# Optimization experiments

Hardware: AMD Instinct MI355X
Metric: run time of the kernel (lower is better)

The kernel has to match this reference:

```python
import jax, jax.numpy as jnp
import numpy as np
from jax import lax

NUM_GROUPS = 16
EPS = 1e-5  # PyTorch GroupNorm default
POOL = 2
CLAMP_MIN, CLAMP_MAX = 0.0, 1.0


def setup_inputs() -> dict:
    key = jax.random.key(0)
    ks = jax.random.split(key, 6)
    B, Cin, H, W = 32, 64, 128, 128
    Cout, K = 128, 3
    return {
        "x": jax.random.normal(ks[0], (B, Cin, H, W), dtype=jnp.float32),
        "conv_w": jax.random.normal(ks[1], (Cout, Cin, K, K), dtype=jnp.float32),
        "conv_b": jax.random.normal(ks[2], (Cout,), dtype=jnp.float32),
        "gn_w": jax.random.normal(ks[3], (Cout,), dtype=jnp.float32),
        "gn_b": jax.random.normal(ks[4], (Cout,), dtype=jnp.float32),
        "scale": jax.random.normal(ks[5], (Cout, 1, 1), dtype=jnp.float32),
    }


def reference(x, conv_w, conv_b, gn_w, gn_b, scale):
    # Conv2d, stride 1, no padding (PyTorch default): [B,Cout,H-2,W-2]
    y = lax.conv_general_dilated(
        x, conv_w, window_strides=(1, 1), padding="VALID",
        dimension_numbers=("NCHW", "OIHW", "NCHW"))
    y = y + conv_b[None, :, None, None]

    # GroupNorm over (C/G, H, W) per sample and group
    B, C, H, W = y.shape
    yg = y.reshape(B, NUM_GROUPS, C // NUM_GROUPS, H, W)
    mean = jnp.mean(yg, axis=(2, 3, 4), keepdims=True)
    var = jnp.var(yg, axis=(2, 3, 4), keepdims=True)
    yn = ((yg - mean) * lax.rsqrt(var + EPS)).reshape(B, C, H, W)
    yn = yn * gn_w[None, :, None, None] + gn_b[None, :, None, None]

    # channel-wise scale (scale shape [C,1,1])
    yn = yn * scale[None, :, :, :]

    # MaxPool2d(kernel=2, stride=2)
    p = lax.reduce_window(yn, -jnp.inf, lax.max,
                          (1, 1, POOL, POOL), (1, 1, POOL, POOL), "VALID")

    # clamp
    return jnp.clip(p, CLAMP_MIN, CLAMP_MAX)
```

## Files before the change

kernel.cpp:

```cpp
#include <hip/hip_runtime.h>
#include <hip/hip_fp16.h>

#define CIN   64
#define COUT  128
#define HIN   128
#define WIN   128
#define HOUT  126
#define WOUT  126
#define HP    63
#define WP    63
#define NB    32
#define NG    16
#define EPS   1e-5f
#define KTOT  576

#define CELLB 80
#define NCOLT 66
#define ROWB  (NCOLT * CELLB)
#define XHALF (4 * ROWB)
#define NTILE 126

#define YCHUNK 128
#define YPLANE (126 * YCHUNK)

typedef __attribute__((ext_vector_type(8))) _Float16 half8;
typedef __attribute__((ext_vector_type(4))) float f32x4;

__global__ __launch_bounds__(256) void wprep_kernel(
    const float* __restrict__ cw, ushort* __restrict__ wh, ushort* __restrict__ wl)
{
    int idx = blockIdx.x * 256 + threadIdx.x;
    if (idx >= COUT * KTOT) return;
    int co = idx / KTOT, k = idx - co * KTOT;
    int khw = k >> 6, ci = k & 63;
    float v = cw[(co * CIN + ci) * 9 + khw];
    __half h = __float2half(v);
    __half l = __float2half(v - __half2float(h));
    wh[idx] = __half_as_ushort(h);
    wl[idx] = __half_as_ushort(l);
}

__global__ __launch_bounds__(512, 4) void conv_mfma_kernel(
    const float* __restrict__ x, const ushort* __restrict__ wt_hi,
    const ushort* __restrict__ wt_lo, const float* __restrict__ cb,
    float* __restrict__ y, float* __restrict__ partials)
{
    __shared__ char xs[2 * XHALF];
    __shared__ float wred[8][4][2];

    const int tid = threadIdx.x;
    const int bid = blockIdx.x;
    const int w   = (bid & 7) * 504 + (bid >> 3);
    const int b   = w / 126;
    const int r   = w - b * 126;
    const int rp  = r >> 1;
    const int ct  = r & 1;
    const int r0x = rp * 2;

    const int l = tid & 63, wid = tid >> 6;
    const int l15 = l & 15, lhi = l >> 4;

    f32x4 acc[8];
#pragma unroll
    for (int nt = 0; nt < 8; ++nt) acc[nt] = (f32x4){0.f, 0.f, 0.f, 0.f};

    const float* xb = x + (size_t)b * (CIN * HIN * WIN);

    const int c4 = tid & 15, rr = (tid >> 4) & 3, cig = tid >> 6;
    const float* xmain = xb + (size_t)(cig * 4) * (HIN * WIN)
                       + (r0x + rr) * WIN + ct * 64 + c4 * 4;
    char* wmain = xs + rr * ROWB + (c4 * 4) * CELLB + cig * 8;

#define LOADMAIN(cip, f)                                                   \
    {                                                                      \
        _Pragma("unroll")                                                  \
        for (int q = 0; q < 4; ++q)                                        \
            f[q] = *(const f32x4*)(xmain + (size_t)((cip) * 32 + q) * (HIN * WIN)); \
    }

#define WRITEMAIN(f, buf)                                                  \
    {                                                                      \
        _Pragma("unroll")                                                  \
        for (int j = 0; j < 4; ++j) {                                      \
            ushort h0 = __half_as_ushort(__float2half(f[0][j]));           \
            ushort h1 = __half_as_ushort(__float2half(f[1][j]));           \
            ushort h2 = __half_as_ushort(__float2half(f[2][j]));           \
            ushort h3 = __half_as_ushort(__float2half(f[3][j]));           \
            uint2 hp;                                                      \
            hp.x = (unsigned)h0 | ((unsigned)h1 << 16);                    \
            hp.y = (unsigned)h2 | ((unsigned)h3 << 16);                    \
            *(uint2*)(wmain + (buf) * XHALF + j * CELLB) = hp;             \
        }                                                                  \
    }

#define TAIL(cip, buf)                                                     \
    if (tid < 32) {                                                        \
        int trr = tid & 3, tcig = tid >> 2;                                \
        float2 g[4];                                                       \
        _Pragma("unroll")                                                  \
        for (int q = 0; q < 4; ++q) {                                      \
            if (ct == 0)                                                   \
                g[q] = *(const float2*)(xb                                 \
                      + (size_t)((cip) * 32 + tcig * 4 + q) * (HIN * WIN)  \
                      + (r0x + trr) * WIN + 64);                           \
            else g[q] = make_float2(0.f, 0.f);                             \
        }                                                                  \
        _Pragma("unroll")                                                  \
        for (int j = 0; j < 2; ++j) {                                      \
            float v0 = j ? g[0].y : g[0].x, v1 = j ? g[1].y : g[1].x;      \
            float v2 = j ? g[2].y : g[2].x, v3 = j ? g[3].y : g[3].x;      \
            uint2 hp;                                                      \
            hp.x = (unsigned)__half_as_ushort(__float2half(v0))            \
                 | ((unsigned)__half_as_ushort(__float2half(v1)) << 16);   \
            hp.y = (unsigned)__half_as_ushort(__float2half(v2))            \
                 | ((unsigned)__half_as_ushort(__float2half(v3)) << 16);   \
            *(uint2*)(xs + (buf) * XHALF + trr * ROWB + (64 + j) * CELLB   \
                      + tcig * 8) = hp;                                    \
        }                                                                  \
    }

    const ushort* wbh = wt_hi + (size_t)(wid * 16 + l15) * KTOT + lhi * 8;
    const ushort* wbl = wt_lo + (size_t)(wid * 16 + l15) * KTOT + lhi * 8;
    const char* pb = xs + l15 * CELLB + lhi * 16;

#define COMPUTE(buf, cip)                                                  \
    {                                                                      \
        _Pragma("unroll")                                                  \
        for (int khw = 0; khw < 9; ++khw) {                                \
            const int kh = khw / 3, kw = khw - kh * 3;                     \
            half8 wh_ = *(const half8*)(wbh + khw * 64 + (cip) * 32);      \
            half8 wl_ = *(const half8*)(wbl + khw * 64 + (cip) * 32);      \
            half8 bv[8];                                                   \
            _Pragma("unroll")                                              \
            for (int nt = 0; nt < 8; ++nt)                                 \
                bv[nt] = *(const half8*)(pb + (buf) * XHALF                \
                        + ((nt >> 2) + kh) * ROWB                          \
                        + ((nt & 3) * 16 + kw) * CELLB);                   \
            _Pragma("unroll")                                              \
            for (int nt = 0; nt < 8; ++nt)                                 \
                acc[nt] = __builtin_amdgcn_mfma_f32_16x16x32_f16(          \
                    wh_, bv[nt], acc[nt], 0, 0, 0);                        \
            _Pragma("unroll")                                              \
            for (int nt = 0; nt < 8; ++nt)                                 \
                acc[nt] = __builtin_amdgcn_mfma_f32_16x16x32_f16(          \
                    wl_, bv[nt], acc[nt], 0, 0, 0);                        \
        }                                                                  \
    }

    {
        f32x4 f0[4];
        LOADMAIN(0, f0);
        WRITEMAIN(f0, 0);
        TAIL(0, 0);
    }
    __syncthreads();

    {
        f32x4 f1[4];
        LOADMAIN(1, f1);
        __builtin_amdgcn_sched_barrier(0);
        COMPUTE(0, 0);
        WRITEMAIN(f1, 1);
        TAIL(1, 1);
    }
    __syncthreads();
    COMPUTE(1, 1);

#undef LOADMAIN
#undef WRITEMAIN
#undef TAIL
#undef COMPUTE

    float cbv[4];
#pragma unroll
    for (int r2 = 0; r2 < 4; ++r2)
        cbv[r2] = cb[wid * 16 + lhi * 4 + r2];

    float* ybase = y + (size_t)b * COUT * YPLANE
                 + (size_t)((rp * 2 + ct) * YCHUNK) + l15;

    float s1 = 0.f, s2 = 0.f;
#pragma unroll
    for (int r2 = 0; r2 < 4; ++r2) {
        int co = wid * 16 + lhi * 4 + r2;
        float* yp = ybase + (size_t)co * YPLANE;
#pragma unroll
        for (int nt = 0; nt < 8; ++nt) {
            float v = acc[nt][r2] + cbv[r2];
            yp[(nt >> 2) * 64 + (nt & 3) * 16] = v;
            if (ct * 64 + (nt & 3) * 16 + l15 < WOUT) { s1 += v; s2 += v * v; }
        }
    }
#pragma unroll
    for (int d = 1; d < 16; d <<= 1) {
        s1 += __shfl_xor(s1, d);
        s2 += __shfl_xor(s2, d);
    }
    if (l15 == 0) {
        wred[wid][lhi][0] = s1;
        wred[wid][lhi][1] = s2;
    }
    __syncthreads();

    if (tid < NG) {
        int g = tid;
        int gw = g >> 1, h = g & 1;
        float t1 = wred[gw][h * 2][0] + wred[gw][h * 2 + 1][0];
        float t2 = wred[gw][h * 2][1] + wred[gw][h * 2 + 1][1];
        size_t pidx = (((size_t)b * NG + g) * NTILE + (rp * 2 + ct)) * 2;
        partials[pidx + 0] = t1;
        partials[pidx + 1] = t2;
    }
}

__global__ void stats_kernel(const float* __restrict__ partials,
                             float* __restrict__ stats)
{
    int t = blockIdx.x * blockDim.x + threadIdx.x;
    if (t >= NB * NG) return;
    float s1 = 0.f, s2 = 0.f;
    for (int j = 0; j < NTILE; ++j) {
        s1 += partials[((size_t)t * NTILE + j) * 2 + 0];
        s2 += partials[((size_t)t * NTILE + j) * 2 + 1];
    }
    const float N = 8.f * HOUT * WOUT;
    float mean = s1 / N;
    float var = s2 / N - mean * mean;
    stats[t * 2 + 0] = mean;
    stats[t * 2 + 1] = rsqrtf(var + EPS);
}

__global__ __launch_bounds__(256) void pool_kernel(
    const float* __restrict__ y, const float* __restrict__ stats,
    const float* __restrict__ gw, const float* __restrict__ gb,
    const float* __restrict__ sc, float* __restrict__ out)
{
    int idx = blockIdx.x * 256 + threadIdx.x;
    if (idx >= NB * COUT * HP * WP) return;
    int owp = idx % WP;
    int t = idx / WP;
    int ohp = t % HP; t /= HP;
    int c = t % COUT;
    int b = t / COUT;
    int g = c >> 3;

    float mean = stats[(b * NG + g) * 2 + 0];
    float rstd = stats[(b * NG + g) * 2 + 1];
    float ga = rstd * gw[c] * sc[c];
    float gbb = (gb[c] - mean * rstd * gw[c]) * sc[c];

    int ct = owp >> 5, col = (2 * owp) & 63;
    const float* yp = y + (size_t)(b * COUT + c) * YPLANE
                    + (ohp * 2 + ct) * YCHUNK + col;
    float2 r0 = *reinterpret_cast<const float2*>(yp);
    float2 r1 = *reinterpret_cast<const float2*>(yp + 64);
    float v0 = fmaf(r0.x, ga, gbb);
    float v1 = fmaf(r0.y, ga, gbb);
    float v2 = fmaf(r1.x, ga, gbb);
    float v3 = fmaf(r1.y, ga, gbb);
    float m = fmaxf(fmaxf(v0, v1), fmaxf(v2, v3));
    out[idx] = fminf(fmaxf(m, 0.f), 1.f);
}

extern "C" void kernel_launch(void* const* d_in, const int* in_sizes, int n_in,
                              void* d_out, int out_size, void* d_ws, size_t ws_size,
                              hipStream_t stream)
{
    const float* x  = (const float*)d_in[0];
    const float* cw = (const float*)d_in[1];
    const float* cbias = (const float*)d_in[2];
    const float* gw = (const float*)d_in[3];
    const float* gb = (const float*)d_in[4];
    const float* sc = (const float*)d_in[5];
    float* out = (float*)d_out;

    const size_t YSZ = (size_t)NB * COUT * YPLANE;
    float* y        = (float*)d_ws;
    float* partials = y + YSZ;
    float* stats    = partials + (size_t)NB * NG * NTILE * 2;
    ushort* wh      = (ushort*)(stats + 1024);
    ushort* wl      = wh + (size_t)COUT * KTOT;

    hipLaunchKernelGGL(wprep_kernel, dim3((COUT * KTOT + 255) / 256), dim3(256),
                       0, stream, cw, wh, wl);

    hipLaunchKernelGGL(conv_mfma_kernel, dim3(4032), dim3(512), 0, stream,
                       x, wh, wl, cbias, y, partials);

    hipLaunchKernelGGL(stats_kernel, dim3(2), dim3(256), 0, stream,
                       partials, stats);

    int total = NB * COUT * HP * WP;
    hipLaunchKernelGGL(pool_kernel, dim3((total + 255) / 256), dim3(256), 0, stream,
                       y, stats, gw, gb, sc, out);
}
```

Measured before the change: 285.8 us.

## Switch conv MFMA from 16x16x32 to 32x32x16 tiles with regrouped warps

Each wavefront now computes a 32-output-channel by 32-column tile with two 32x32x16 f16 MFMA accumulators (one per output row), replacing eight 16x16x32 accumulators. Waves are paired so each pair shares a channel group and splits the columns. The epilogue remaps the output layout and reduces GroupNorm partial sums per 8-channel group across the whole wave. The aim is to cut LDS operand loads per MFMA and make the matrix cores more efficient; the risk is a different LDS bank-access pattern and extra shuffle reductions.

New measurement: 397.9 us. 39.2% more time.

```diff
diff --git a/kernel.cpp b/kernel.cpp
--- a/kernel.cpp
+++ b/kernel.cpp
@@ -23,8 +23,9 @@
 #define YCHUNK 128
 #define YPLANE (126 * YCHUNK)
 
-typedef __attribute__((ext_vector_type(8))) _Float16 half8;
-typedef __attribute__((ext_vector_type(4))) float f32x4;
+typedef __attribute__((ext_vector_type(8)))  _Float16 half8;
+typedef __attribute__((ext_vector_type(4)))  float f32x4;
+typedef __attribute__((ext_vector_type(16))) float f32x16;
 
 __global__ __launch_bounds__(256) void wprep_kernel(
     const float* __restrict__ cw, ushort* __restrict__ wh, ushort* __restrict__ wl)
@@ -58,11 +59,13 @@
     const int r0x = rp * 2;
 
     const int l = tid & 63, wid = tid >> 6;
-    const int l15 = l & 15, lhi = l >> 4;
-
-    f32x4 acc[8];
-#pragma unroll
-    for (int nt = 0; nt < 8; ++nt) acc[nt] = (f32x4){0.f, 0.f, 0.f, 0.f};
+    const int wg = wid >> 1;
+    const int h  = wid & 1;
+    const int l31 = l & 31, lh = l >> 5;
+
+    f32x16 acc0 = (f32x16){0.f,0.f,0.f,0.f,0.f,0.f,0.f,0.f,
+                           0.f,0.f,0.f,0.f,0.f,0.f,0.f,0.f};
+    f32x16 acc1 = acc0;
 
     const float* xb = x + (size_t)b * (CIN * HIN * WIN);
 
@@ -119,31 +122,28 @@
         }                                                                  \
     }
 
-    const ushort* wbh = wt_hi + (size_t)(wid * 16 + l15) * KTOT + lhi * 8;
-    const ushort* wbl = wt_lo + (size_t)(wid * 16 + l15) * KTOT + lhi * 8;
-    const char* pb = xs + l15 * CELLB + lhi * 16;
+    const ushort* wbh = wt_hi + (size_t)(wg * 32 + l31) * KTOT + lh * 8;
+    const ushort* wbl = wt_lo + (size_t)(wg * 32 + l31) * KTOT + lh * 8;
+    const char* pb = xs + (h * 32 + l31) * CELLB + lh * 16;
 
 #define COMPUTE(buf, cip)                                                  \
     {                                                                      \
         _Pragma("unroll")                                                  \
         for (int khw = 0; khw < 9; ++khw) {                                \
             const int kh = khw / 3, kw = khw - kh * 3;                     \
-            half8 wh_ = *(const half8*)(wbh + khw * 64 + (cip) * 32);      \
-            half8 wl_ = *(const half8*)(wbl + khw * 64 + (cip) * 32);      \
-            half8 bv[8];                                                   \
             _Pragma("unroll")                                              \
-            for (int nt = 0; nt < 8; ++nt)                                 \
-                bv[nt] = *(const half8*)(pb + (buf) * XHALF                \
-                        + ((nt >> 2) + kh) * ROWB                          \
-                        + ((nt & 3) * 16 + kw) * CELLB);                   \
-            _Pragma("unroll")                                              \
-            for (int nt = 0; nt < 8; ++nt)                                 \
-                acc[nt] = __builtin_amdgcn_mfma_f32_16x16x32_f16(          \
-                    wh_, bv[nt], acc[nt], 0, 0, 0);                        \
-            _Pragma("unroll")                                              \
-            for (int nt = 0; nt < 8; ++nt)                                 \
-                acc[nt] = __builtin_amdgcn_mfma_f32_16x16x32_f16(          \
-                    wl_, bv[nt], acc[nt], 0, 0, 0);                        \
+            for (int k16 = 0; k16 < 2; ++k16) {                            \
+                half8 wh_ = *(const half8*)(wbh + khw * 64 + (cip) * 32 + k16 * 16); \
+                half8 wl_ = *(const half8*)(wbl + khw * 64 + (cip) * 32 + k16 * 16); \
+                half8 bv0 = *(const half8*)(pb + (buf) * XHALF             \
+                            + kh * ROWB + kw * CELLB + k16 * 32);          \
+                half8 bv1 = *(const half8*)(pb + (buf) * XHALF             \
+                            + (1 + kh) * ROWB + kw * CELLB + k16 * 32);    \
+                acc0 = __builtin_amdgcn_mfma_f32_32x32x16_f16(wh_, bv0, acc0, 0, 0, 0); \
+                acc1 = __builtin_amdgcn_mfma_f32_32x32x16_f16(wh_, bv1, acc1, 0, 0, 0); \
+                acc0 = __builtin_amdgcn_mfma_f32_32x32x16_f16(wl_, bv0, acc0, 0, 0, 0); \
+                acc1 = __builtin_amdgcn_mfma_f32_32x32x16_f16(wl_, bv1, acc1, 0, 0, 0); \
+            }                                                              \
         }                                                                  \
     }
 
@@ -171,42 +171,45 @@
 #undef TAIL
 #undef COMPUTE
 
-    float cbv[4];
+    float* ybase = y + (size_t)b * COUT * YPLANE + (size_t)((rp * 2 + ct) * YCHUNK);
+    const bool okcol = (ct * 64 + h * 32 + l31) < WOUT;
+
+    float s1g[4] = {0.f, 0.f, 0.f, 0.f};
+    float s2g[4] = {0.f, 0.f, 0.f, 0.f};
 #pragma unroll
-    for (int r2 = 0; r2 < 4; ++r2)
-        cbv[r2] = cb[wid * 16 + lhi * 4 + r2];
-
-    float* ybase = y + (size_t)b * COUT * YPLANE
-                 + (size_t)((rp * 2 + ct) * YCHUNK) + l15;
-
-    float s1 = 0.f, s2 = 0.f;
+    for (int j = 0; j < 16; ++j) {
+        int co = wg * 32 + (j & 3) + 4 * lh + 8 * (j >> 2);
+        float bias = cb[co];
+        float* yp = ybase + (size_t)co * YPLANE + h * 32 + l31;
+        float v0 = acc0[j] + bias;
+        float v1 = acc1[j] + bias;
+        yp[0]  = v0;
+        yp[64] = v1;
+        if (okcol) {
+            s1g[j >> 2] += v0 + v1;
+            s2g[j >> 2] += v0 * v0 + v1 * v1;
+        }
+    }
 #pragma unroll
-    for (int r2 = 0; r2 < 4; ++r2) {
-        int co = wid * 16 + lhi * 4 + r2;
-        float* yp = ybase + (size_t)co * YPLANE;
+    for (int g2 = 0; g2 < 4; ++g2) {
+        float a = s1g[g2], q = s2g[g2];
 #pragma unroll
-        for (int nt = 0; nt < 8; ++nt) {
-            float v = acc[nt][r2] + cbv[r2];
-            yp[(nt >> 2) * 64 + (nt & 3) * 16] = v;
-            if (ct * 64 + (nt & 3) * 16 + l15 < WOUT) { s1 += v; s2 += v * v; }
+        for (int d = 1; d < 64; d <<= 1) {
+            a += __shfl_xor(a, d);
+            q += __shfl_xor(q, d);
         }
-    }
-#pragma unroll
-    for (int d = 1; d < 16; d <<= 1) {
-        s1 += __shfl_xor(s1, d);
-        s2 += __shfl_xor(s2, d);
-    }
-    if (l15 == 0) {
-        wred[wid][lhi][0] = s1;
-        wred[wid][lhi][1] = s2;
+        if (l == 0) {
+            wred[wid][g2][0] = a;
+            wred[wid][g2][1] = q;
+        }
     }
     __syncthreads();
 
     if (tid < NG) {
         int g = tid;
-        int gw = g >> 1, h = g & 1;
-        float t1 = wred[gw][h * 2][0] + wred[gw][h * 2 + 1][0];
-        float t2 = wred[gw][h * 2][1] + wred[gw][h * 2 + 1][1];
+        int wg2 = g >> 2, g2 = g & 3;
+        float t1 = wred[wg2 * 2][g2][0] + wred[wg2 * 2 + 1][g2][0];
+        float t2 = wred[wg2 * 2][g2][1] + wred[wg2 * 2 + 1][g2][1];
         size_t pidx = (((size_t)b * NG + g) * NTILE + (rp * 2 + ct)) * 2;
         partials[pidx + 0] = t1;
         partials[pidx + 1] = t2;
```

## Retile conv MFMA warps to 32 channels by 4 pixel tiles

Applied to the files above, without the earlier changes.

Each wavefront now computes 2 output-channel tiles by 4 pixel tiles instead of 1 channel tile by 8 pixel tiles, with wave pairs splitting the columns. This halves the LDS B-fragment reads per MFMA while doubling the per-wave weight loads from global/cache. The GroupNorm partial-sum reduction is rearranged to match the new channel/column ownership.

Result: slower. 422.9 us (+48.0%).

```diff
diff --git a/kernel.cpp b/kernel.cpp
--- a/kernel.cpp
+++ b/kernel.cpp
@@ -46,7 +46,7 @@
     float* __restrict__ y, float* __restrict__ partials)
 {
     __shared__ char xs[2 * XHALF];
-    __shared__ float wred[8][4][2];
+    __shared__ float wred[8][2][4][2];
 
     const int tid = threadIdx.x;
     const int bid = blockIdx.x;
@@ -58,11 +58,16 @@
     const int r0x = rp * 2;
 
     const int l = tid & 63, wid = tid >> 6;
+    const int wg = wid >> 1;
+    const int h  = wid & 1;
     const int l15 = l & 15, lhi = l >> 4;
 
-    f32x4 acc[8];
-#pragma unroll
-    for (int nt = 0; nt < 8; ++nt) acc[nt] = (f32x4){0.f, 0.f, 0.f, 0.f};
+    f32x4 acc[2][4];
+#pragma unroll
+    for (int mt = 0; mt < 2; ++mt)
+#pragma unroll
+        for (int nt = 0; nt < 4; ++nt)
+            acc[mt][nt] = (f32x4){0.f, 0.f, 0.f, 0.f};
 
     const float* xb = x + (size_t)b * (CIN * HIN * WIN);
 
@@ -119,8 +124,8 @@
         }                                                                  \
     }
 
-    const ushort* wbh = wt_hi + (size_t)(wid * 16 + l15) * KTOT + lhi * 8;
-    const ushort* wbl = wt_lo + (size_t)(wid * 16 + l15) * KTOT + lhi * 8;
+    const ushort* wbh = wt_hi + (size_t)(wg * 32 + l15) * KTOT + lhi * 8;
+    const ushort* wbl = wt_lo + (size_t)(wg * 32 + l15) * KTOT + lhi * 8;
     const char* pb = xs + l15 * CELLB + lhi * 16;
 
 #define COMPUTE(buf, cip)                                                  \
@@ -128,22 +133,30 @@
         _Pragma("unroll")                                                  \
         for (int khw = 0; khw < 9; ++khw) {                                \
             const int kh = khw / 3, kw = khw - kh * 3;                     \
-            half8 wh_ = *(const half8*)(wbh + khw * 64 + (cip) * 32);      \
-            half8 wl_ = *(const half8*)(wbl + khw * 64 + (cip) * 32);      \
-            half8 bv[8];                                                   \
+            half8 ah[2], al[2];                                            \
             _Pragma("unroll")                                              \
-            for (int nt = 0; nt < 8; ++nt)                                 \
+            for (int mt = 0; mt < 2; ++mt) {                               \
+                ah[mt] = *(const half8*)(wbh + mt * 16 * KTOT + khw * 64 + (cip) * 32); \
+                al[mt] = *(const half8*)(wbl + mt * 16 * KTOT + khw * 64 + (cip) * 32); \
+            }                                                              \
+            half8 bv[4];                                                   \
+            _Pragma("unroll")                                              \
+            for (int nt = 0; nt < 4; ++nt)                                 \
                 bv[nt] = *(const half8*)(pb + (buf) * XHALF                \
-                        + ((nt >> 2) + kh) * ROWB                          \
-                        + ((nt & 3) * 16 + kw) * CELLB);                   \
+                        + ((nt >> 1) + kh) * ROWB                          \
+                        + (h * 32 + (nt & 1) * 16 + kw) * CELLB);          \
             _Pragma("unroll")                                              \
-            for (int nt = 0; nt < 8; ++nt)                                 \
-                acc[nt] = __builtin_amdgcn_mfma_f32_16x16x32_f16(          \
-                    wh_, bv[nt], acc[nt], 0, 0, 0);                        \
+            for (int mt = 0; mt < 2; ++mt)                                 \
+                _Pragma("unroll")                                          \
+                for (int nt = 0; nt < 4; ++nt)                             \
+                    acc[mt][nt] = __builtin_amdgcn_mfma_f32_16x16x32_f16(  \
+                        ah[mt], bv[nt], acc[mt][nt], 0, 0, 0);             \
             _Pragma("unroll")                                              \
-            for (int nt = 0; nt < 8; ++nt)                                 \
-                acc[nt] = __builtin_amdgcn_mfma_f32_16x16x32_f16(          \
-                    wl_, bv[nt], acc[nt], 0, 0, 0);                        \
+            for (int mt = 0; mt < 2; ++mt)                                 \
+                _Pragma("unroll")                                          \
+                for (int nt = 0; nt < 4; ++nt)                             \
+                    acc[mt][nt] = __builtin_amdgcn_mfma_f32_16x16x32_f16(  \
+                        al[mt], bv[nt], acc[mt][nt], 0, 0, 0);             \
         }                                                                  \
     }
 
@@ -171,42 +184,49 @@
 #undef TAIL
 #undef COMPUTE
 
-    float cbv[4];
-#pragma unroll
-    for (int r2 = 0; r2 < 4; ++r2)
-        cbv[r2] = cb[wid * 16 + lhi * 4 + r2];
-
     float* ybase = y + (size_t)b * COUT * YPLANE
-                 + (size_t)((rp * 2 + ct) * YCHUNK) + l15;
-
-    float s1 = 0.f, s2 = 0.f;
-#pragma unroll
-    for (int r2 = 0; r2 < 4; ++r2) {
-        int co = wid * 16 + lhi * 4 + r2;
-        float* yp = ybase + (size_t)co * YPLANE;
-#pragma unroll
-        for (int nt = 0; nt < 8; ++nt) {
-            float v = acc[nt][r2] + cbv[r2];
-            yp[(nt >> 2) * 64 + (nt & 3) * 16] = v;
-            if (ct * 64 + (nt & 3) * 16 + l15 < WOUT) { s1 += v; s2 += v * v; }
+                 + (size_t)((rp * 2 + ct) * YCHUNK) + h * 32 + l15;
+
+#pragma unroll
+    for (int mt = 0; mt < 2; ++mt) {
+        float s1 = 0.f, s2 = 0.f;
+#pragma unroll
+        for (int r2 = 0; r2 < 4; ++r2) {
+            int co = wg * 32 + mt * 16 + lhi * 4 + r2;
+            float bias = cb[co];
+            float* yp = ybase + (size_t)co * YPLANE;
+#pragma unroll
+            for (int nt = 0; nt < 4; ++nt) {
+                float v = acc[mt][nt][r2] + bias;
+                yp[(nt >> 1) * 64 + (nt & 1) * 16] = v;
+                if (ct * 64 + h * 32 + (nt & 1) * 16 + l15 < WOUT) {
+                    s1 += v; s2 += v * v;
+                }
+            }
         }
-    }
-#pragma unroll
-    for (int d = 1; d < 16; d <<= 1) {
-        s1 += __shfl_xor(s1, d);
-        s2 += __shfl_xor(s2, d);
-    }
-    if (l15 == 0) {
-        wred[wid][lhi][0] = s1;
-        wred[wid][lhi][1] = s2;
+#pragma unroll
+        for (int d = 1; d < 16; d <<= 1) {
+            s1 += __shfl_xor(s1, d);
+            s2 += __shfl_xor(s2, d);
+        }
+        if (l15 == 0) {
+            wred[wid][mt][lhi][0] = s1;
+            wred[wid][mt][lhi][1] = s2;
+        }
     }
     __syncthreads();
 
     if (tid < NG) {
         int g = tid;
-        int gw = g >> 1, h = g & 1;
-        float t1 = wred[gw][h * 2][0] + wred[gw][h * 2 + 1][0];
-        float t2 = wred[gw][h * 2][1] + wred[gw][h * 2 + 1][1];
+        int wg2 = g >> 2, mt = (g >> 1) & 1, lh0 = (g & 1) * 2;
+        float t1 = 0.f, t2 = 0.f;
+#pragma unroll
+        for (int hh = 0; hh < 2; ++hh)
+#pragma unroll
+            for (int dl = 0; dl < 2; ++dl) {
+                t1 += wred[wg2 * 2 + hh][mt][lh0 + dl][0];
+                t2 += wred[wg2 * 2 + hh][mt][lh0 + dl][1];
+            }
         size_t pidx = (((size_t)b * NG + g) * NTILE + (rp * 2 + ct)) * 2;
         partials[pidx + 0] = t1;
         partials[pidx + 1] = t2;
```
